# Kernel optimization log

Measured on AMD Instinct MI355X. Metric: run time of the kernel, lower is better.

## Reference

```python
import jax, jax.numpy as jnp
import numpy as np

B, T, N, M, P, YD = 256, 64, 128, 256, 256, 1


def lstm_cell(x, h, c, Wih, Whh, bih, bhh):
    # torch LSTM gate order: i, f, g, o
    gates = x @ Wih.T + h @ Whh.T + bih + bhh  # (B, 4H)
    i, f, g, o = jnp.split(gates, 4, axis=-1)
    c_new = jax.nn.sigmoid(f) * c + jax.nn.sigmoid(i) * jnp.tanh(g)
    h_new = jax.nn.sigmoid(o) * jnp.tanh(c_new)
    return h_new, c_new


def setup_inputs() -> dict:
    key = jax.random.key(0)
    ks = jax.random.split(key, 20)
    s = 0.05
    return {
        "inputs": jax.random.normal(ks[0], (B, T, N + YD), jnp.float32),
        "WU_e": jax.random.normal(ks[1], (T, 2 * M + T), jnp.float32) * s,
        "v_e": jax.random.normal(ks[2], (1, T), jnp.float32) * s,
        "Wih_e": jax.random.normal(ks[3], (4 * M, N), jnp.float32) * s,
        "Whh_e": jax.random.normal(ks[4], (4 * M, M), jnp.float32) * s,
        "bih_e": jax.random.normal(ks[5], (4 * M,), jnp.float32) * s,
        "bhh_e": jax.random.normal(ks[6], (4 * M,), jnp.float32) * s,
        "WU_d": jax.random.normal(ks[7], (M, 2 * P + M), jnp.float32) * s,
        "v_d": jax.random.normal(ks[8], (1, M), jnp.float32) * s,
        "wb_tilde": jax.random.normal(ks[9], (1, YD + M), jnp.float32) * s,
        "Wih_d": jax.random.normal(ks[10], (4 * P, 1), jnp.float32) * s,
        "Whh_d": jax.random.normal(ks[11], (4 * P, P), jnp.float32) * s,
        "bih_d": jax.random.normal(ks[12], (4 * P,), jnp.float32) * s,
        "bhh_d": jax.random.normal(ks[13], (4 * P,), jnp.float32) * s,
        "Wb_W": jax.random.normal(ks[14], (P, P + M), jnp.float32) * s,
        "Wb_b": jax.random.normal(ks[15], (P,), jnp.float32) * s,
        "vb_W": jax.random.normal(ks[16], (YD, P), jnp.float32) * s,
        "vb_b": jax.random.normal(ks[17], (YD,), jnp.float32) * s,
    }


def _darnn(inputs, WU_e, v_e, Wih_e, Whh_e, bih_e, bhh_e,
           WU_d, v_d, wb_tilde, Wih_d, Whh_d, bih_d, bhh_d,
           Wb_W, Wb_b, vb_W, vb_b):
    X = inputs[:, :, :N]          # (B, T, N)
    Y = inputs[:, :, N:]          # (B, T, YD)
    X_nt = jnp.transpose(X, (0, 2, 1))  # (B, N, T), constant across encoder steps

    # ---------------- Encoder ----------------
    def enc_step(carry, x_t):  # x_t: (B, N)
        h, c = carry
        hs = jnp.concatenate([h, c], axis=-1)  # (B, 2M)
        feat = jnp.concatenate(
            [jnp.broadcast_to(hs[:, None, :], (B, N, 2 * M)), X_nt], axis=-1)  # (B, N, 2M+T)
        E = (jnp.tanh(feat @ WU_e.T) @ v_e.T)[..., 0]  # (B, N)
        alpha = jax.nn.softmax(E, axis=1)
        h, c = lstm_cell(x_t * alpha, h, c, Wih_e, Whh_e, bih_e, bhh_e)
        return (h, c), h

    h0 = jnp.zeros((B, M), inputs.dtype)
    c0 = jnp.zeros((B, M), inputs.dtype)
    _, X_encoded = jax.lax.scan(enc_step, (h0, c0), jnp.transpose(X, (1, 0, 2)))
    Xe_bm = jnp.transpose(X_encoded, (1, 0, 2))  # (B, T, M)

    # ---------------- Decoder ----------------
    def dec_step(carry, y_t):  # y_t: (B, YD)
        h, c, _ = carry
        hs = jnp.concatenate([h, c], axis=-1)  # (B, 2P)
        feat = jnp.concatenate(
            [jnp.broadcast_to(hs[:, None, :], (B, T, 2 * P)), Xe_bm], axis=-1)  # (B, T, 2P+M)
        l = (jnp.tanh(feat @ WU_d.T) @ v_d.T)[..., 0]  # (B, T)
        beta = jax.nn.softmax(l, axis=1)
        ctx = jnp.einsum('bt,btm->bm', beta, Xe_bm)  # (B, M)
        y_tilde = jnp.concatenate([y_t, ctx], axis=-1) @ wb_tilde.T  # (B, 1)
        h, c = lstm_cell(y_tilde, h, c, Wih_d, Whh_d, bih_d, bhh_d)
        return (h, c, ctx), None

    hd0 = jnp.zeros((B, P), inputs.dtype)
    cd0 = jnp.zeros((B, P), inputs.dtype)
    ctx0 = jnp.zeros((B, M), inputs.dtype)
    (h, c, ctx), _ = jax.lax.scan(
        dec_step, (hd0, cd0, ctx0), jnp.transpose(Y[:, :T - 1, :], (1, 0, 2)))

    hidden = jnp.concatenate([h, ctx], axis=-1) @ Wb_W.T + Wb_b  # (B, P)
    y_hat = hidden @ vb_W.T + vb_b  # (B, YD)
    return y_hat


def reference(inputs, WU_e, v_e, Wih_e, Whh_e, bih_e, bhh_e,
              WU_d, v_d, wb_tilde, Wih_d, Whh_d, bih_d, bhh_d,
              Wb_W, Wb_b, vb_W, vb_b):
    return _darnn(inputs, WU_e, v_e, Wih_e, Whh_e, bih_e, bhh_e,
                  WU_d, v_d, wb_tilde, Wih_d, Whh_d, bih_d, bhh_d,
                  Wb_W, Wb_b, vb_W, vb_b)
```

## Files before the change

kernel.cpp:

```cpp
#include <hip/hip_runtime.h>
#include <math.h>


#define OFF_XWT   0u
#define OFF_XEWT  2097152u
#define OFF_XE    6291456u
#define OFF_HE    10485760u
#define OFF_HD    10616832u
#define OFF_SB    10747904u
#define OFF_SDB   10780672u
#define OFF_XA    10911744u
#define OFF_CTX   10944512u
#define OFF_YT    11010048u
#define OFF_BAR   11010304u
#define WS_END    11010816u

#define SENT_U 0x7FC00001u

#define SLAB_F 24576
#define PER_F  2432
#define SCR_F  12288
#define FLG_F  16
#define SMEM_F (SLAB_F + PER_F + SCR_F + FLG_F)
#define SMEM_BYTES (SMEM_F * 4)

#define F_E 0
#define F_L 1
#define F_B 2

__device__ __forceinline__ float fast_tanh(float x) {
  float xc = fminf(15.f, fmaxf(-15.f, x));
  float e = __expf(2.f * xc);
  return 1.f - 2.f * __builtin_amdgcn_rcpf(e + 1.f);
}
__device__ __forceinline__ float fast_sig(float x) {
  float xc = fminf(30.f, fmaxf(-30.f, x));
  return __builtin_amdgcn_rcpf(1.f + __expf(-xc));
}
__device__ __forceinline__ float wave_max(float v) {
#pragma unroll
  for (int o = 32; o; o >>= 1) v = fmaxf(v, __shfl_xor(v, o));
  return v;
}
__device__ __forceinline__ float wave_sum(float v) {
#pragma unroll
  for (int o = 32; o; o >>= 1) v += __shfl_xor(v, o);
  return v;
}
__device__ __forceinline__ float dot4(float4 a, float4 b) {
  return a.x*b.x + a.y*b.y + a.z*b.z + a.w*b.w;
}

__device__ __forceinline__ void st1_sc1(float* p, float v) {
  asm volatile("global_store_dword %0, %1, off sc1" :: "v"(p), "v"(v) : "memory");
}
__device__ __forceinline__ void ld1q_sc1(float4& a, const float* pa) {
  asm volatile("global_load_dwordx4 %0, %1, off sc1\n\ts_waitcnt vmcnt(0)"
               : "=&v"(a) : "v"(pa) : "memory");
}
__device__ __forceinline__ void ld1q_nw(float4& a, const float* pa) {
  asm volatile("global_load_dwordx4 %0, %1, off sc1"
               : "=&v"(a) : "v"(pa) : "memory");
}
__device__ __forceinline__ void vm0() {
  asm volatile("s_waitcnt vmcnt(0)" ::: "memory");
}
__device__ __forceinline__ void lgk0() {
  asm volatile("s_waitcnt lgkmcnt(0)" ::: "memory");
}
__device__ __forceinline__ float ld1s_sc1(const float* p) {
  float v;
  asm volatile("global_load_dword %0, %1, off sc1\n\ts_waitcnt vmcnt(0)"
               : "=&v"(v) : "v"(p) : "memory");
  return v;
}
__device__ __forceinline__ void ld8s_sc1(
    float& a0,float& a1,float& a2,float& a3,float& a4,float& a5,float& a6,float& a7,
    const float* p0,const float* p1,const float* p2,const float* p3,
    const float* p4,const float* p5,const float* p6,const float* p7) {
  asm volatile(
      "global_load_dword %0, %8, off sc1\n\t"
      "global_load_dword %1, %9, off sc1\n\t"
      "global_load_dword %2, %10, off sc1\n\t"
      "global_load_dword %3, %11, off sc1\n\t"
      "global_load_dword %4, %12, off sc1\n\t"
      "global_load_dword %5, %13, off sc1\n\t"
      "global_load_dword %6, %14, off sc1\n\t"
      "global_load_dword %7, %15, off sc1\n\t"
      "s_waitcnt vmcnt(0)"
      : "=&v"(a0),"=&v"(a1),"=&v"(a2),"=&v"(a3),
        "=&v"(a4),"=&v"(a5),"=&v"(a6),"=&v"(a7)
      : "v"(p0),"v"(p1),"v"(p2),"v"(p3),"v"(p4),"v"(p5),"v"(p6),"v"(p7)
      : "memory");
}

__device__ __forceinline__ void lds_inc(unsigned* f) {
  __hip_atomic_fetch_add(f, 1u, __ATOMIC_RELAXED, __HIP_MEMORY_SCOPE_WORKGROUP);
}
__device__ __forceinline__ void lds_poll(unsigned* f, unsigned tgt) {
  unsigned cur;
  do { cur = __hip_atomic_load(f, __ATOMIC_RELAXED, __HIP_MEMORY_SCOPE_WORKGROUP); } while (cur < tgt);
  asm volatile("" ::: "memory");
}

#define FMA16V(a0,a1,a2,a3,xv,wv) \
  a0.x += xv.x*wv.x; a0.y += xv.x*wv.y; a0.z += xv.x*wv.z; a0.w += xv.x*wv.w; \
  a1.x += xv.y*wv.x; a1.y += xv.y*wv.y; a1.z += xv.y*wv.z; a1.w += xv.y*wv.w; \
  a2.x += xv.z*wv.x; a2.y += xv.z*wv.y; a2.z += xv.z*wv.z; a2.w += xv.z*wv.w; \
  a3.x += xv.w*wv.x; a3.y += xv.w*wv.y; a3.z += xv.w*wv.z; a3.w += xv.w*wv.w;

__device__ __forceinline__ void bar_arrive(unsigned* bar) {
  asm volatile("s_waitcnt vmcnt(0)" ::: "memory");
  __syncthreads();
  if (threadIdx.x == 0)
    __hip_atomic_fetch_add(bar, 1u, __ATOMIC_RELAXED, __HIP_MEMORY_SCOPE_AGENT);
}
__device__ __forceinline__ void bar_wait(unsigned* bar, unsigned target) {
  if (threadIdx.x == 0) {
    unsigned cur;
    do {
      __builtin_amdgcn_s_sleep(1);
      cur = __hip_atomic_load(bar, __ATOMIC_RELAXED, __HIP_MEMORY_SCOPE_AGENT);
    } while (cur < target);
  }
  __syncthreads();
}

__global__ void darnn_init(float* __restrict__ ws, float* __restrict__ out) {
  unsigned i = blockIdx.x * 256u + threadIdx.x;
  const unsigned span = WS_END - OFF_HE;
  for (unsigned idx = i; idx < span; idx += gridDim.x * 256u) ws[OFF_HE + idx] = 0.f;
  for (unsigned idx = i; idx < 262144u; idx += gridDim.x * 256u) {
    unsigned g = idx >> 14, off = idx & 16383u;
    ws[OFF_XEWT + g * 262144u + off] = 0.f;
  }
  if (i < 256u) out[i] = 0.f;
}

__global__ __launch_bounds__(512, 2) void darnn_main(
    const float* __restrict__ in,   const float* __restrict__ WUe,   const float* __restrict__ ve,
    const float* __restrict__ Wih_e,const float* __restrict__ Whh_e,
    const float* __restrict__ bih_e,const float* __restrict__ bhh_e,
    const float* __restrict__ WUd,  const float* __restrict__ vd,
    const float* __restrict__ wbt,  const float* __restrict__ Wih_d,
    const float* __restrict__ Whh_d,const float* __restrict__ bih_d, const float* __restrict__ bhh_d,
    const float* __restrict__ WbW,  const float* __restrict__ Wbb,
    const float* __restrict__ vbW,  const float* __restrict__ vbb,
    float* __restrict__ ws, float* __restrict__ out)
{
  extern __shared__ __align__(16) float sm[];
  float* SLAB = sm;
  float* PER  = sm + SLAB_F;
  float* SCR  = sm + SLAB_F + PER_F;
  unsigned* FLG = (unsigned*)(sm + SLAB_F + PER_F + SCR_F);
  const int tid = threadIdx.x;
  const int bid = blockIdx.x;
  const int grp = bid >> 4;
  const int mt  = bid & 15;
  const int b0  = grp << 4;
  const float SENTF = __uint_as_float(SENT_U);

  float* XWt  = ws + OFF_XWT;
  float* XeWt = ws + OFF_XEWT;
  float* Xe   = ws + OFF_XE;
  float* EP = ws + OFF_XEWT + (unsigned)grp * 262144u;
  float* DP = ws + OFF_XWT  + (unsigned)grp * 131072u;
  unsigned* barp = (unsigned*)(ws + OFF_BAR) + grp * 32;
  unsigned barn = 0;

  if (tid < FLG_F) FLG[tid] = 0u;

  float* wue_s  = PER;
  float* ve_s   = PER + 2304;
  float* bsum_e = PER + 2368;

  const int jfixE = ((tid & 63) + mt * 4) & 63;

  {
    int r = tid & 63, kq = tid >> 6;
    int grow = (r & 3) * 256 + mt * 16 + (r >> 2);
#pragma unroll 4
    for (int q = 0; q < 12; ++q) {
      int k = kq * 48 + q * 4;
      float4 wv = (k < 128) ? *(const float4*)(Wih_e + grow * 128 + k)
                            : *(const float4*)(Whh_e + grow * 256 + (k - 128));
      SLAB[(k + 0) * 64 + r] = wv.x; SLAB[(k + 1) * 64 + r] = wv.y;
      SLAB[(k + 2) * 64 + r] = wv.z; SLAB[(k + 3) * 64 + r] = wv.w;
    }
    {
      int lin = tid * 4;
      int j = lin >> 5, c0 = lin & 31;
      int col = (c0 < 16) ? (mt * 16 + c0) : (256 + mt * 16 + (c0 - 16));
      float4 wv = *(const float4*)(WUe + j * 576 + col);
      *(float4*)(wue_s + j * 36 + c0) = wv;
    }
    if (tid < 64) {
      ve_s[tid] = ve[tid];
      int g = tid >> 4, m2 = tid & 15, m = mt * 16 + m2;
      bsum_e[tid] = bih_e[g * 256 + m] + bhh_e[g * 256 + m];
    }
  }

  {
    float* Xs = SCR;
    const float* Xb = in + bid * 8256;
    __syncthreads();
    for (int it = 0; it < 16; ++it) {
      int lin = tid + it * 512;
      int k = lin >> 7, n = lin & 127;
      Xs[n * 68 + k] = Xb[k * 129 + n];
    }
    __syncthreads();
    int j = tid & 63, nh = tid >> 6;
    float acc[16];
#pragma unroll
    for (int i = 0; i < 16; ++i) acc[i] = 0.f;
    const float* wrow = WUe + j * 576 + 512;
    for (int kc = 0; kc < 4; ++kc) {
      float4 w0 = *(const float4*)(wrow + kc * 16 + 0);
      float4 w1 = *(const float4*)(wrow + kc * 16 + 4);
      float4 w2 = *(const float4*)(wrow + kc * 16 + 8);
      float4 w3 = *(const float4*)(wrow + kc * 16 + 12);
#pragma unroll
      for (int ni = 0; ni < 16; ++ni) {
        const float* xp = Xs + (nh * 16 + ni) * 68 + kc * 16;
        acc[ni] += dot4(*(const float4*)(xp + 0),  w0) + dot4(*(const float4*)(xp + 4),  w1)
                 + dot4(*(const float4*)(xp + 8),  w2) + dot4(*(const float4*)(xp + 12), w3);
      }
    }
    float* dst = XWt + bid * 8192 + j * 128 + nh * 16;
#pragma unroll
    for (int ni = 0; ni < 16; ++ni) dst[ni] = acc[ni];
    __syncthreads();
  }

  float4 whc[8];
#pragma unroll
  for (int q = 0; q < 8; ++q) whc[q] = *(const float4*)(wue_s + jfixE * 36 + q * 4);
  float4 bsE = {0,0,0,0};
  {
    int m2 = tid & 15;
    bsE.x = bsum_e[m2]; bsE.y = bsum_e[16 + m2];
    bsE.z = bsum_e[32 + m2]; bsE.w = bsum_e[48 + m2];
  }
  float xwreg[32];
  if (tid < 256) {
    int w = tid >> 6, l = tid & 63;
    const float* xwp = XWt + bid * 8192;
#pragma unroll
    for (int jj = 0; jj < 16; ++jj) {
      xwreg[jj]      = xwp[(w * 16 + jj) * 128 + l];
      xwreg[16 + jj] = xwp[(w * 16 + jj) * 128 + 64 + l];
    }
  }
  float c_reg = 0.f;

  for (int t = 0; t < 64; ++t) {
    const int rd = t & 1, wr2 = (t + 1) & 1;
    float* xah = SCR + 1024;
    const int ks = tid >> 6, ml = (tid >> 2) & 15, b4 = tid & 3;
    float4 a0 = {0,0,0,0}, a1 = {0,0,0,0}, a2 = {0,0,0,0}, a3 = {0,0,0,0};

    bar_wait(barp, barn);

    if (tid < 256) {
      int w = tid >> 6, l = tid & 63;
      float* Sj = SCR;
      float* Ep = SCR + 64;
      {
        float4 s;
        ld1q_sc1(s, EP + (unsigned)rd * 16384u + (unsigned)mt * 1024u
                       + (unsigned)((l >> 2) * 64 + w * 16 + (l & 3) * 4));
#pragma unroll
        for (int off = 4; off <= 32; off <<= 1) {
          s.x += __shfl_xor(s.x, off);
          s.y += __shfl_xor(s.y, off);
          s.z += __shfl_xor(s.z, off);
          s.w += __shfl_xor(s.w, off);
        }
        if (l < 4) *(float4*)(Sj + w * 16 + l * 4) = s;
        lgk0();
      }
      float e0 = 0.f, e1 = 0.f;
#pragma unroll
      for (int jj = 0; jj < 16; ++jj) {
        float s = Sj[w * 16 + jj];
        float vv = ve_s[w * 16 + jj];
        e0 += vv * fast_tanh(xwreg[jj] + s);
        e1 += vv * fast_tanh(xwreg[16 + jj] + s);
      }
      Ep[w * 128 + l] = e0;
      Ep[w * 128 + 64 + l] = e1;
      lgk0();
      if (l == 0) lds_inc(FLG + F_E);
      if (w == 0) {
        lds_poll(FLG + F_E, 4u * (t + 1));
        float En0 = Ep[l] + Ep[128 + l] + Ep[256 + l] + Ep[384 + l];
        float En1 = Ep[64 + l] + Ep[192 + l] + Ep[320 + l] + Ep[448 + l];
        float mx = wave_max(fmaxf(En0, En1));
        float ex0 = __expf(En0 - mx), ex1 = __expf(En1 - mx);
        float tot = wave_sum(ex0 + ex1);
        float rt = __builtin_amdgcn_rcpf(tot);
        float x0 = in[bid * 8256 + t * 129 + l];
        float x1 = in[bid * 8256 + t * 129 + 64 + l];
        float* XAg = ws + OFF_XA + (unsigned)grp * 2048;
        st1_sc1(XAg + l * 16 + mt, x0 * ex0 * rt);
        st1_sc1(XAg + (64 + l) * 16 + mt, x1 * ex1 * rt);
        vm0();
        if (tid == 0)
          __hip_atomic_fetch_add(barp, 1u, __ATOMIC_RELAXED, __HIP_MEMORY_SCOPE_AGENT);
      }
    } else {
      int u = tid - 256;
      float4 h0, h1, h2, h3;
      const float* hb = ws + OFF_HE + (unsigned)rd * 65536 + (unsigned)grp * 4096 + u * 16;
      ld1q_nw(h0, hb); ld1q_nw(h1, hb + 4); ld1q_nw(h2, hb + 8); ld1q_nw(h3, hb + 12);
      vm0();
      float* row = xah + (unsigned)(128 + u) * 20;
      *(float4*)(row + 0) = h0; *(float4*)(row + 4) = h1;
      *(float4*)(row + 8) = h2; *(float4*)(row + 12) = h3;
      lgk0();
      int s = u >> 6;
      const float* xp = xah + (unsigned)(128 + s * 64) * 20 + b4 * 4;
      const float* wp = SLAB + (unsigned)(128 + s * 64) * 64 + ml * 4;
#pragma unroll 8
      for (int kk = 0; kk < 64; ++kk) {
        float4 xv = *(const float4*)(xp + kk * 20);
        float4 wv = *(const float4*)(wp + kk * 64);
        FMA16V(a0, a1, a2, a3, xv, wv);
      }
    }
    barn += 16;
    bar_wait(barp, barn);

    if (t == 63 && tid == 0) {
      float* sp = ws + OFF_SB + 16384u + (unsigned)bid * 64u;
      st1_sc1(sp + 0, SENTF); st1_sc1(sp + 1, SENTF);
    }
    {
      int l = tid & 63;
      int k = (ks << 4) + (l >> 2), i4 = (l & 3) * 4;
      float4 q;
      ld1q_sc1(q, ws + OFF_XA + (unsigned)grp * 2048 + k * 16 + i4);
      *(float4*)(xah + k * 20 + i4) = q;
      lgk0();
    }
    {
      const float* xp = xah + (unsigned)(ks * 16) * 20 + b4 * 4;
      const float* wp = SLAB + (unsigned)(ks * 16) * 64 + ml * 4;
#pragma unroll 8
      for (int kk = 0; kk < 16; ++kk) {
        float4 xv = *(const float4*)(xp + kk * 20);
        float4 wv = *(const float4*)(wp + kk * 64);
        FMA16V(a0, a1, a2, a3, xv, wv);
      }
    }
    __syncthreads();
    float* red = SCR;
    {
      float* rp = red + (unsigned)(ks * 64 + ml * 4 + b4) * 20;
      *(float4*)(rp + 0) = a0; *(float4*)(rp + 4) = a1;
      *(float4*)(rp + 8) = a2; *(float4*)(rp + 12) = a3;
    }
    __syncthreads();
    float* hcs = SCR + 10240;
    if (tid < 256) {
      int m2 = tid & 15, bl = tid >> 4;
      int t2 = m2 * 4 + (bl >> 2), bs = bl & 3;
      float4 gate = {0,0,0,0};
#pragma unroll
      for (int k2 = 0; k2 < 8; ++k2) {
        float4 rr = *(const float4*)(red + (unsigned)(k2 * 64 + t2) * 20 + bs * 4);
        gate.x += rr.x; gate.y += rr.y; gate.z += rr.z; gate.w += rr.w;
      }
      float gi = gate.x + bsE.x, gf = gate.y + bsE.y;
      float gg = gate.z + bsE.z, go = gate.w + bsE.w;
      float cn = fast_sig(gf) * c_reg + fast_sig(gi) * fast_tanh(gg);
      float hn = fast_sig(go) * fast_tanh(cn);
      c_reg = cn;
      unsigned m = mt * 16 + m2;
      st1_sc1(ws + OFF_HE + (unsigned)wr2 * 65536 + (unsigned)grp * 4096 + m * 16 + bl, hn);
      st1_sc1(Xe + ((unsigned)(b0 + bl) * 64 + t) * 256 + m, hn);
      hcs[bl * 32 + m2] = hn;
      hcs[bl * 32 + 16 + m2] = cn;
    }
    __syncthreads();
    {
      int wq = tid >> 6;
#pragma unroll
      for (int e2 = 0; e2 < 2; ++e2) {
        int bl2 = wq * 2 + e2;
        const float* hp = hcs + bl2 * 32;
        float s = 0.f;
#pragma unroll
        for (int q = 0; q < 4; ++q) {
          s += dot4(*(const float4*)(hp + q * 4), whc[q]);
          s += dot4(*(const float4*)(hp + 16 + q * 4), whc[4 + q]);
        }
        st1_sc1(EP + (unsigned)wr2 * 16384u + (unsigned)bl2 * 1024u
                   + (unsigned)mt * 64u + (unsigned)jfixE, s);
      }
    }
    barn += 16;
    bar_arrive(barp);
  }
  bar_wait(barp, barn);

  float xe[64];
  if (tid < 256) {
    const float* xb = Xe + (unsigned)bid * 16384 + tid;
#pragma unroll
    for (int g8 = 0; g8 < 8; ++g8) {
      ld8s_sc1(xe[g8*8+0], xe[g8*8+1], xe[g8*8+2], xe[g8*8+3],
               xe[g8*8+4], xe[g8*8+5], xe[g8*8+6], xe[g8*8+7],
               xb + (g8*8+0)*256, xb + (g8*8+1)*256, xb + (g8*8+2)*256,
               xb + (g8*8+3)*256, xb + (g8*8+4)*256, xb + (g8*8+5)*256,
               xb + (g8*8+6)*256, xb + (g8*8+7)*256);
    }
  }

  float* vd_s   = PER;
  float* wbt_s  = PER + 256;
  float* bsum_d = PER + 520;
  float* wihd_s = PER + 584;
  float* q_s    = PER + 704;
  float* qpart  = PER + 768;
  float* wudT   = SLAB + 16384;
  const int jfixD = ((tid & 255) + mt * 16) & 255;
  __syncthreads();
  {
    int r = tid & 63, kq = tid >> 6;
    int grow = (r & 3) * 256 + mt * 16 + (r >> 2);
#pragma unroll 4
    for (int q = 0; q < 8; ++q) {
      int k = kq * 32 + q * 4;
      float4 wv = *(const float4*)(Whh_d + grow * 256 + k);
      SLAB[(k + 0) * 64 + r] = wv.x; SLAB[(k + 1) * 64 + r] = wv.y;
      SLAB[(k + 2) * 64 + r] = wv.z; SLAB[(k + 3) * 64 + r] = wv.w;
    }
    {
      int j = tid & 255, half = tid >> 8;
#pragma unroll
      for (int i = 0; i < 16; ++i) {
        int c = half * 16 + i;
        int col = (c < 16) ? (mt * 16 + c) : (256 + mt * 16 + (c - 16));
        wudT[c * 256 + j] = WUd[(unsigned)j * 768 + col];
      }
    }
    if (tid < 256) vd_s[tid] = vd[tid];
    if (tid < 257) wbt_s[tid] = wbt[tid];
    if (tid < 64) {
      int g = tid >> 4, m2 = tid & 15, m = mt * 16 + m2;
      bsum_d[tid] = bih_d[g * 256 + m] + bhh_d[g * 256 + m];
      wihd_s[tid] = Wih_d[g * 256 + m];
    }
  }
  __syncthreads();

  if (tid < 256) {
    int w = tid >> 6, l = tid & 63;
    float wm = wbt_s[1 + tid];
#pragma unroll
    for (int t4 = 0; t4 < 64; ++t4) {
      float v = wave_sum(wm * xe[t4]);
      if (l == 0) qpart[w * 64 + t4] = v;
    }
  }
  __syncthreads();
  if (tid < 64) q_s[tid] = qpart[tid] + qpart[64 + tid] + qpart[128 + tid] + qpart[192 + tid];
  __syncthreads();

  {
    float* XeT = SCR;
    float* Wdc = SCR + 4096;
    int tt2 = tid & 15, jq = tid >> 4;
    for (int jc = 0; jc < 2; ++jc) {
      float4 c0 = {0,0,0,0}, c1 = {0,0,0,0}, c2 = {0,0,0,0}, c3 = {0,0,0,0};
      for (int kc = 0; kc < 4; ++kc) {
        __syncthreads();
        if (tid < 256 && (tid >> 6) == kc) {
          int kk = tid & 63;
#pragma unroll
          for (int t4 = 0; t4 < 16; ++t4) {
            float4 v = { xe[t4*4+0], xe[t4*4+1], xe[t4*4+2], xe[t4*4+3] };
            *(float4*)(XeT + kk * 64 + t4 * 4) = v;
          }
        }
        {
          int jj = tid >> 2, k16 = (tid & 3) * 16;
          const float* src = WUd + (unsigned)(jc * 128 + jj) * 768 + 512 + kc * 64 + k16;
#pragma unroll
          for (int s4 = 0; s4 < 4; ++s4) {
            float4 wv = *(const float4*)(src + s4 * 4);
            Wdc[(k16 + s4*4 + 0) * 128 + jj] = wv.x;
            Wdc[(k16 + s4*4 + 1) * 128 + jj] = wv.y;
            Wdc[(k16 + s4*4 + 2) * 128 + jj] = wv.z;
            Wdc[(k16 + s4*4 + 3) * 128 + jj] = wv.w;
          }
        }
        __syncthreads();
#pragma unroll 8
        for (int kk = 0; kk < 64; ++kk) {
          float4 xv = *(const float4*)(XeT + kk * 64 + tt2 * 4);
          float4 wv = *(const float4*)(Wdc + kk * 128 + jq * 4);
          FMA16V(c0, c1, c2, c3, wv, xv);
        }
      }
      int jb = jc * 128 + jq * 4;
      *(float4*)(XeWt + ((unsigned)bid * 256 + jb + 0) * 64 + tt2 * 4) = c0;
      *(float4*)(XeWt + ((unsigned)bid * 256 + jb + 1) * 64 + tt2 * 4) = c1;
      *(float4*)(XeWt + ((unsigned)bid * 256 + jb + 2) * 64 + tt2 * 4) = c2;
      *(float4*)(XeWt + ((unsigned)bid * 256 + jb + 3) * 64 + tt2 * 4) = c3;
    }
    __syncthreads();
  }

  float wreg[32];
#pragma unroll
  for (int c = 0; c < 32; ++c) wreg[c] = wudT[c * 256 + jfixD];
  float4 bsD = {0,0,0,0}, wiD = {0,0,0,0};
  {
    int m2 = tid & 15;
    bsD.x = bsum_d[m2]; bsD.y = bsum_d[16 + m2]; bsD.z = bsum_d[32 + m2]; bsD.w = bsum_d[48 + m2];
    wiD.x = wihd_s[m2]; wiD.y = wihd_s[16 + m2]; wiD.z = wihd_s[32 + m2]; wiD.w = wihd_s[48 + m2];
  }
  float xewreg[64];
  if (tid < 256) {
    int w = tid >> 6, l = tid & 63;
    const float* xew = XeWt + (unsigned)bid * 16384 + l;
#pragma unroll
    for (int jj = 0; jj < 64; ++jj) xewreg[jj] = xew[(w * 64 + jj) << 6];
  }
  float q_reg = 0.f, yv = 0.f;
  if (tid < 64) {
    q_reg = q_s[tid];
    if (tid < 63) yv = in[bid * 8256 + tid * 129 + 128];
  }
  const float wbt0 = wbt_s[0];
  float cd_reg = 0.f;

  {
    float* dp0 = DP + (unsigned)mt * 4096u;
#pragma unroll
    for (int i8 = 0; i8 < 8; ++i8) st1_sc1(dp0 + (unsigned)(i8 * 512 + tid), 0.f);
    barn += 16;
    bar_arrive(barp);
  }

  for (int t = 0; t < 63; ++t) {
    const int rd = t & 1, wr2 = (t + 1) & 1;
    const int ml = (tid >> 2) & 15, b4 = tid & 3;
    float* hT  = SCR + 2048;
    float* red = SCR + 7168;

    bar_wait(barp, barn);

    if (tid < 256) {
      int w = tid >> 6, l = tid & 63;
      float* Sdj  = SCR;
      float* lp   = SCR + 256;
      float* beta = SCR + 512;
      {
        int jq = (l & 15) * 4, mq = l >> 4;
        const float* dpb = DP + (unsigned)rd * 65536u + (unsigned)mt * 4096u
                              + (unsigned)(w * 64 + jq);
        float4 p0, p1, p2, p3;
        ld1q_nw(p0, dpb + (unsigned)((mq +  0) * 256));
        ld1q_nw(p1, dpb + (unsigned)((mq +  4) * 256));
        ld1q_nw(p2, dpb + (unsigned)((mq +  8) * 256));
        ld1q_nw(p3, dpb + (unsigned)((mq + 12) * 256));
        vm0();
        float4 s;
        s.x = (p0.x + p1.x) + (p2.x + p3.x);
        s.y = (p0.y + p1.y) + (p2.y + p3.y);
        s.z = (p0.z + p1.z) + (p2.z + p3.z);
        s.w = (p0.w + p1.w) + (p2.w + p3.w);
#pragma unroll
        for (int off = 16; off <= 32; off <<= 1) {
          s.x += __shfl_xor(s.x, off);
          s.y += __shfl_xor(s.y, off);
          s.z += __shfl_xor(s.z, off);
          s.w += __shfl_xor(s.w, off);
        }
        if (mq == 0) *(float4*)(Sdj + w * 64 + jq) = s;
        lgk0();
      }
      float lpar = 0.f;
#pragma unroll 8
      for (int jj = 0; jj < 64; ++jj)
        lpar += vd_s[w * 64 + jj] * fast_tanh(xewreg[jj] + Sdj[w * 64 + jj]);
      lp[w * 64 + l] = lpar;
      lgk0();
      if (l == 0) lds_inc(FLG + F_L);
      if (w == 0) {
        lds_poll(FLG + F_L, 4u * (t + 1));
        float lv = lp[l] + lp[64 + l] + lp[128 + l] + lp[192 + l];
        float mx = wave_max(lv);
        float ex = __expf(lv - mx);
        float sw = wave_sum(ex);
        float rt = __builtin_amdgcn_rcpf(sw);
        float ytn = wave_sum(ex * q_reg);
        if (l == 0) {
          float yt = wbt0 * __shfl(yv, t) + ytn * rt;
          st1_sc1(ws + OFF_SB + 16384u + (unsigned)bid * 64u + (unsigned)rd, yt);
        }
        if (t == 62) {
          beta[l] = ex * rt;
          lgk0();
          if (l == 0) lds_inc(FLG + F_B);
        }
      }
      if (t == 62) {
        lds_poll(FLG + F_B, 1u);
        lgk0();
        float ctx = 0.f;
#pragma unroll
        for (int tt = 0; tt < 64; ++tt) ctx += beta[tt] * xe[tt];
        st1_sc1(ws + OFF_CTX + (unsigned)bid * 256 + tid, ctx);
      }
    } else {
      if (tid == 256)
        st1_sc1(ws + OFF_SB + 16384u + (unsigned)bid * 64u + (unsigned)wr2, SENTF);
      int u = tid - 256;
      float4 h0, h1, h2, h3;
      const float* hb = ws + OFF_HD + (unsigned)rd * 65536 + (unsigned)grp * 4096 + u * 16;
      ld1q_nw(h0, hb); ld1q_nw(h1, hb + 4); ld1q_nw(h2, hb + 8); ld1q_nw(h3, hb + 12);
      vm0();
      float* row = hT + (unsigned)u * 20;
      *(float4*)(row + 0) = h0; *(float4*)(row + 4) = h1;
      *(float4*)(row + 8) = h2; *(float4*)(row + 12) = h3;
      lgk0();
      int s = u >> 6;
      float4 a0 = {0,0,0,0}, a1 = {0,0,0,0}, a2 = {0,0,0,0}, a3 = {0,0,0,0};
      const float* xp = hT + (unsigned)(s * 64) * 20 + b4 * 4;
      const float* wp = SLAB + (unsigned)(s * 64) * 64 + ml * 4;
#pragma unroll 8
      for (int kk = 0; kk < 64; ++kk) {
        float4 xv = *(const float4*)(xp + kk * 20);
        float4 wv = *(const float4*)(wp + kk * 64);
        FMA16V(a0, a1, a2, a3, xv, wv);
      }
      float* rp = red + (unsigned)(s * 64 + ml * 4 + b4) * 20;
      *(float4*)(rp + 0) = a0; *(float4*)(rp + 4) = a1;
      *(float4*)(rp + 8) = a2; *(float4*)(rp + 12) = a3;
    }
    __syncthreads();

    float* hcs = SCR;
    if (tid < 256) {
      int m2 = tid & 15, bl = tid >> 4;
      int t2 = m2 * 4 + (bl >> 2), bs = bl & 3;
      float4 gate = {0,0,0,0};
#pragma unroll
      for (int k2 = 0; k2 < 4; ++k2) {
        float4 rr = *(const float4*)(red + (unsigned)(k2 * 64 + t2) * 20 + bs * 4);
        gate.x += rr.x; gate.y += rr.y; gate.z += rr.z; gate.w += rr.w;
      }
      const float* pyt = ws + OFF_SB + 16384u + (unsigned)(b0 + bl) * 64u + (unsigned)rd;
      float yt_reg = ld1s_sc1(pyt);
      while (__float_as_uint(yt_reg) == SENT_U) {
        __builtin_amdgcn_s_sleep(4);
        yt_reg = ld1s_sc1(pyt);
      }
      float gi = gate.x + yt_reg * wiD.x + bsD.x;
      float gf = gate.y + yt_reg * wiD.y + bsD.y;
      float gg = gate.z + yt_reg * wiD.z + bsD.z;
      float go = gate.w + yt_reg * wiD.w + bsD.w;
      float cn = fast_sig(gf) * cd_reg + fast_sig(gi) * fast_tanh(gg);
      float hn = fast_sig(go) * fast_tanh(cn);
      cd_reg = cn;
      unsigned m = mt * 16 + m2;
      st1_sc1(ws + OFF_HD + (unsigned)wr2 * 65536 + (unsigned)grp * 4096 + m * 16 + bl, hn);
      hcs[bl * 32 + m2] = hn;
      hcs[bl * 32 + 16 + m2] = cn;
    }
    __syncthreads();
    {
      int half = tid >> 8;
#pragma unroll
      for (int e2 = 0; e2 < 8; ++e2) {
        int bl2 = half * 8 + e2;
        const float* hp = hcs + bl2 * 32;
        float s = 0.f;
#pragma unroll
        for (int c = 0; c < 16; ++c) s += hp[c] * wreg[c];
#pragma unroll
        for (int c = 0; c < 16; ++c) s += hp[16 + c] * wreg[16 + c];
        st1_sc1(DP + (unsigned)wr2 * 65536u + (unsigned)bl2 * 4096u
                   + (unsigned)mt * 256u + (unsigned)jfixD, s);
      }
    }
    barn += 16;
    bar_arrive(barp);
  }
  bar_wait(barp, barn);

  {
    float* hsf  = SCR;
    float* hid2 = SCR + 8256;
    {
      int l0 = tid * 2, l1 = tid * 2 + 1;
      int k0 = l0 >> 2, i0 = l0 & 3, k1 = l1 >> 2, i1 = l1 & 3;
      const float* hb = ws + OFF_HD + 65536u + (unsigned)grp * 4096;
      int bl0 = l0 >> 6, c0 = (l0 & 63) * 4, bl1 = l1 >> 6, c1 = (l1 & 63) * 4;
      float4 qa, qb, qc, qd;
      ld1q_nw(qa, hb + k0 * 16 + i0 * 4);
      ld1q_nw(qb, hb + k1 * 16 + i1 * 4);
      ld1q_nw(qc, ws + OFF_CTX + (unsigned)(b0 + bl0) * 256 + c0);
      ld1q_nw(qd, ws + OFF_CTX + (unsigned)(b0 + bl1) * 256 + c1);
      vm0();
      hsf[(i0 * 4 + 0) * 516 + k0] = qa.x; hsf[(i0 * 4 + 1) * 516 + k0] = qa.y;
      hsf[(i0 * 4 + 2) * 516 + k0] = qa.z; hsf[(i0 * 4 + 3) * 516 + k0] = qa.w;
      hsf[(i1 * 4 + 0) * 516 + k1] = qb.x; hsf[(i1 * 4 + 1) * 516 + k1] = qb.y;
      hsf[(i1 * 4 + 2) * 516 + k1] = qb.z; hsf[(i1 * 4 + 3) * 516 + k1] = qb.w;
      *(float4*)(hsf + bl0 * 516 + 256 + c0) = qc;
      *(float4*)(hsf + bl1 * 516 + 256 + c1) = qd;
    }
    __syncthreads();
    int bl = tid & 15, p4 = (tid >> 4) & 15, half = tid >> 8;
    int row = mt * 16 + p4;
    const float* wrow = WbW + (unsigned)row * 512 + half * 256;
    const float* hp = hsf + bl * 516 + half * 256;
    float acc = half ? 0.f : Wbb[row];
#pragma unroll 8
    for (int q = 0; q < 64; ++q)
      acc += dot4(*(const float4*)(hp + q * 4), *(const float4*)(wrow + q * 4));
    hid2[half * 272 + bl * 17 + p4] = acc;
    __syncthreads();
    if (tid < 16) {
      float s = 0.f;
#pragma unroll
      for (int p = 0; p < 16; ++p)
        s += (hid2[tid * 17 + p] + hid2[272 + tid * 17 + p]) * vbW[mt * 16 + p];
      if (mt == 0) s += vbb[0];
      atomicAdd(&out[b0 + tid], s);
    }
  }
}

extern "C" void kernel_launch(void* const* d_in, const int* in_sizes, int n_in,
                              void* d_out, int out_size, void* d_ws, size_t ws_size,
                              hipStream_t stream) {
  (void)in_sizes; (void)n_in; (void)out_size; (void)ws_size;
  const float* in    = (const float*)d_in[0];
  const float* WUe   = (const float*)d_in[1];
  const float* ve    = (const float*)d_in[2];
  const float* Wih_e = (const float*)d_in[3];
  const float* Whh_e = (const float*)d_in[4];
  const float* bih_e = (const float*)d_in[5];
  const float* bhh_e = (const float*)d_in[6];
  const float* WUd   = (const float*)d_in[7];
  const float* vd    = (const float*)d_in[8];
  const float* wbt   = (const float*)d_in[9];
  const float* Wih_d = (const float*)d_in[10];
  const float* Whh_d = (const float*)d_in[11];
  const float* bih_d = (const float*)d_in[12];
  const float* bhh_d = (const float*)d_in[13];
  const float* WbW   = (const float*)d_in[14];
  const float* Wbb   = (const float*)d_in[15];
  const float* vbW   = (const float*)d_in[16];
  const float* vbb   = (const float*)d_in[17];
  float* ws  = (float*)d_ws;
  float* out = (float*)d_out;

  (void)hipFuncSetAttribute((const void*)darnn_main,
                            hipFuncAttributeMaxDynamicSharedMemorySize, SMEM_BYTES);
  hipLaunchKernelGGL(darnn_init, dim3(1024), dim3(256), 0, stream, ws, out);
  hipLaunchKernelGGL(darnn_main, dim3(256), dim3(512), SMEM_BYTES, stream,
                     in, WUe, ve, Wih_e, Whh_e, bih_e, bhh_e,
                     WUd, vd, wbt, Wih_d, Whh_d, bih_d, bhh_d,
                     WbW, Wbb, vbW, vbb, ws, out);
}
```

Measured before the change: 1.209 ms.

## Replace atomic group barrier with per-block flag stores and parallel polling

Swaps the agent-scope atomic counter barrier shared by each 16-block group for per-block epoch flags in global memory, written with plain sc1 stores. Sixteen lanes poll the sixteen flags in parallel and combine the result through an LDS counter. Waiting wavefronts poll LDS instead of going through a full __syncthreads. This is meant to remove atomic contention and shorten the hundreds of per-step barriers on the serial encoder and decoder path. The cost is more global polling traffic, and correctness now depends on the flag layout and the monotonic epoch numbering.

Result: no change. 1.200 ms, median of 2 (-0.7%).

```diff
diff --git a/kernel.cpp b/kernel.cpp
--- a/kernel.cpp
+++ b/kernel.cpp
@@ -24,9 +24,11 @@
 #define SMEM_F (SLAB_F + PER_F + SCR_F + FLG_F)
 #define SMEM_BYTES (SMEM_F * 4)
 
-#define F_E 0
-#define F_L 1
-#define F_B 2
+#define F_E   0
+#define F_L   1
+#define F_B   2
+#define F_TOP 3
+#define F_XA  4
 
 __device__ __forceinline__ float fast_tanh(float x) {
   float xc = fminf(15.f, fmaxf(-15.f, x));
@@ -53,6 +55,15 @@
 
 __device__ __forceinline__ void st1_sc1(float* p, float v) {
   asm volatile("global_store_dword %0, %1, off sc1" :: "v"(p), "v"(v) : "memory");
+}
+__device__ __forceinline__ void stu_sc1(unsigned* p, unsigned v) {
+  asm volatile("global_store_dword %0, %1, off sc1" :: "v"(p), "v"(v) : "memory");
+}
+__device__ __forceinline__ unsigned ldu_sc1(const unsigned* p) {
+  unsigned v;
+  asm volatile("global_load_dword %0, %1, off sc1\n\ts_waitcnt vmcnt(0)"
+               : "=&v"(v) : "v"(p) : "memory");
+  return v;
 }
 __device__ __forceinline__ void ld1q_sc1(float4& a, const float* pa) {
   asm volatile("global_load_dwordx4 %0, %1, off sc1\n\ts_waitcnt vmcnt(0)"
@@ -103,28 +114,21 @@
   asm volatile("" ::: "memory");
 }
 
+__device__ __forceinline__ void spin16(const unsigned* fl, int idx, unsigned tgt) {
+  const unsigned* p = fl + idx * 16;
+  unsigned v = ldu_sc1(p);
+  while (v < tgt) { __builtin_amdgcn_s_sleep(1); v = ldu_sc1(p); }
+}
+__device__ __forceinline__ void wait_full(const unsigned* fl, unsigned tgt, int tid) {
+  if (tid < 16) spin16(fl, tid, tgt);
+  __syncthreads();
+}
+
 #define FMA16V(a0,a1,a2,a3,xv,wv) \
   a0.x += xv.x*wv.x; a0.y += xv.x*wv.y; a0.z += xv.x*wv.z; a0.w += xv.x*wv.w; \
   a1.x += xv.y*wv.x; a1.y += xv.y*wv.y; a1.z += xv.y*wv.z; a1.w += xv.y*wv.w; \
   a2.x += xv.z*wv.x; a2.y += xv.z*wv.y; a2.z += xv.z*wv.z; a2.w += xv.z*wv.w; \
   a3.x += xv.w*wv.x; a3.y += xv.w*wv.y; a3.z += xv.w*wv.z; a3.w += xv.w*wv.w;
-
-__device__ __forceinline__ void bar_arrive(unsigned* bar) {
-  asm volatile("s_waitcnt vmcnt(0)" ::: "memory");
-  __syncthreads();
-  if (threadIdx.x == 0)
-    __hip_atomic_fetch_add(bar, 1u, __ATOMIC_RELAXED, __HIP_MEMORY_SCOPE_AGENT);
-}
-__device__ __forceinline__ void bar_wait(unsigned* bar, unsigned target) {
-  if (threadIdx.x == 0) {
-    unsigned cur;
-    do {
-      __builtin_amdgcn_s_sleep(1);
-      cur = __hip_atomic_load(bar, __ATOMIC_RELAXED, __HIP_MEMORY_SCOPE_AGENT);
-    } while (cur < target);
-  }
-  __syncthreads();
-}
 
 __global__ void darnn_init(float* __restrict__ ws, float* __restrict__ out) {
   unsigned i = blockIdx.x * 256u + threadIdx.x;
@@ -165,8 +169,8 @@
   float* Xe   = ws + OFF_XE;
   float* EP = ws + OFF_XEWT + (unsigned)grp * 262144u;
   float* DP = ws + OFF_XWT  + (unsigned)grp * 131072u;
-  unsigned* barp = (unsigned*)(ws + OFF_BAR) + grp * 32;
-  unsigned barn = 0;
+  unsigned* FLA = (unsigned*)(ws + OFF_SDB) + (unsigned)grp * 512u;
+  unsigned* FLB = FLA + 256u;
 
   if (tid < FLG_F) FLG[tid] = 0u;
 
@@ -261,7 +265,9 @@
     const int ks = tid >> 6, ml = (tid >> 2) & 15, b4 = tid & 3;
     float4 a0 = {0,0,0,0}, a1 = {0,0,0,0}, a2 = {0,0,0,0}, a3 = {0,0,0,0};
 
-    bar_wait(barp, barn);
+    if (tid >= 64 && tid < 80) spin16(FLA, tid - 64, (unsigned)t);
+    if (tid == 64) lds_inc(FLG + F_TOP);
+    lds_poll(FLG + F_TOP, (unsigned)(t + 1));
 
     if (tid < 256) {
       int w = tid >> 6, l = tid & 63;
@@ -307,8 +313,7 @@
         st1_sc1(XAg + l * 16 + mt, x0 * ex0 * rt);
         st1_sc1(XAg + (64 + l) * 16 + mt, x1 * ex1 * rt);
         vm0();
-        if (tid == 0)
-          __hip_atomic_fetch_add(barp, 1u, __ATOMIC_RELAXED, __HIP_MEMORY_SCOPE_AGENT);
+        if (tid == 0) stu_sc1(FLB + mt * 16, (unsigned)(t + 1));
       }
     } else {
       int u = tid - 256;
@@ -330,8 +335,10 @@
         FMA16V(a0, a1, a2, a3, xv, wv);
       }
     }
-    barn += 16;
-    bar_wait(barp, barn);
+
+    if (tid >= 64 && tid < 80) spin16(FLB, tid - 64, (unsigned)(t + 1));
+    if (tid == 64) lds_inc(FLG + F_XA);
+    lds_poll(FLG + F_XA, (unsigned)(t + 1));
 
     if (t == 63 && tid == 0) {
       float* sp = ws + OFF_SB + 16384u + (unsigned)bid * 64u;
@@ -401,10 +408,11 @@
                    + (unsigned)mt * 64u + (unsigned)jfixE, s);
       }
     }
-    barn += 16;
-    bar_arrive(barp);
-  }
-  bar_wait(barp, barn);
+    vm0();
+    __syncthreads();
+    if (tid == 0) stu_sc1(FLA + mt * 16, (unsigned)(t + 1));
+  }
+  wait_full(FLA, 64u, tid);
 
   float xe[64];
   if (tid < 256) {
@@ -543,8 +551,9 @@
     float* dp0 = DP + (unsigned)mt * 4096u;
 #pragma unroll
     for (int i8 = 0; i8 < 8; ++i8) st1_sc1(dp0 + (unsigned)(i8 * 512 + tid), 0.f);
-    barn += 16;
-    bar_arrive(barp);
+    vm0();
+    __syncthreads();
+    if (tid == 0) stu_sc1(FLA + mt * 16, 65u);
   }
 
   for (int t = 0; t < 63; ++t) {
@@ -553,7 +562,9 @@
     float* hT  = SCR + 2048;
     float* red = SCR + 7168;
 
-    bar_wait(barp, barn);
+    if (tid >= 64 && tid < 80) spin16(FLA, tid - 64, (unsigned)(65 + t));
+    if (tid == 64) lds_inc(FLG + F_TOP);
+    lds_poll(FLG + F_TOP, (unsigned)(65 + t));
 
     if (tid < 256) {
       int w = tid >> 6, l = tid & 63;
@@ -690,10 +701,11 @@
                    + (unsigned)mt * 256u + (unsigned)jfixD, s);
       }
     }
-    barn += 16;
-    bar_arrive(barp);
-  }
-  bar_wait(barp, barn);
+    vm0();
+    __syncthreads();
+    if (tid == 0) stu_sc1(FLA + mt * 16, (unsigned)(66 + t));
+  }
+  wait_full(FLA, 128u, tid);
 
   {
     float* hsf  = SCR;
```
